# Kernel tuning notes

Hardware: AMD Instinct MI355X
Metric: run time of the kernel (lower is better)

## Reference

```python
import jax, jax.numpy as jnp
import numpy as np

EPS = 1e-5  # torch group_norm default
GROUPS = 32


def _nin(t, W, b):
    # torch Nin: einsum('bchw,co->bowh') transposes spatial dims, then adds bias
    return jnp.einsum('bchw,co->bowh', t, W) + b


def setup_inputs() -> dict:
    key = jax.random.key(0)
    ks = jax.random.split(key, 9)
    B, C, N = 16, 512, 32
    x = jax.random.normal(ks[0], (B, C, N, N), jnp.float32)
    sc = 0.02
    Wq = jax.random.normal(ks[1], (C, C), jnp.float32) * sc
    Wk = jax.random.normal(ks[2], (C, C), jnp.float32) * sc
    Wv = jax.random.normal(ks[3], (C, C), jnp.float32) * sc
    Wn = jax.random.normal(ks[4], (C, C), jnp.float32) * sc
    bq = jnp.zeros((1, C, 1, 1), jnp.float32)
    bk = jnp.zeros((1, C, 1, 1), jnp.float32)
    bv = jnp.zeros((1, C, 1, 1), jnp.float32)
    bn = jnp.zeros((1, C, 1, 1), jnp.float32)
    return {"x": x, "Wq": Wq, "bq": bq, "Wk": Wk, "bk": bk,
            "Wv": Wv, "bv": bv, "Wn": Wn, "bn": bn}


def reference(x, Wq, bq, Wk, bk, Wv, bv, Wn, bn):
    B, C, H, W = x.shape
    # GroupNorm(32) with no affine params
    xg = x.reshape(B, GROUPS, -1)
    mu = xg.mean(-1, keepdims=True)
    var = xg.var(-1, keepdims=True)
    h = ((xg - mu) / jnp.sqrt(var + EPS)).reshape(B, C, H, W)
    # Nin projections -> spatially transposed (B, C, W, H)
    q = _nin(h, Wq, bq)
    k = _nin(h, Wk, bk)
    v = _nin(h, Wv, bv)
    # scores s[b,w1,w2,h1,h2] = sum_c q[b,c,w1,h1] k[b,c,w2,h2] * C^-0.5
    s = jnp.einsum('bcwh,bcWH->bwWhH', q, k) * (C ** -0.5)
    # softmax over flat (h1,h2) blocks exactly as the torch reshape does
    s = jax.nn.softmax(s.reshape(B, H, W, H * W), axis=-1).reshape(B, H, W, H, W)
    # torch.einsum('bHWHW, bcWH -> bcWH', w, v) takes the DIAGONAL over the
    # repeated H and W labels: diag[b,i,j] = s[b,i,j,i,j], then elementwise
    # scales v: out[b,c,w,h] = diag[b,h,w] * v[b,c,w,h]
    i = jnp.arange(H)
    j = jnp.arange(W)
    diag = s[:, i[:, None], j[None, :], i[:, None], j[None, :]]  # (B,H,W)
    h2 = v * jnp.swapaxes(diag, 1, 2)[:, None]  # (B,C,W,H)
    out = _nin(h2, Wn, bn)  # transposes back -> (B,C,H,W)
    return x + out
```

## Files before the change

### kernel.cpp

```cpp
#include <hip/hip_runtime.h>
#include <hip/hip_bf16.h>

typedef __attribute__((ext_vector_type(8))) short short8;
typedef __attribute__((ext_vector_type(4))) float floatx4;

#define MFMA16(a, b, c) __builtin_amdgcn_mfma_f32_16x16x32_bf16((a), (b), (c), 0, 0, 0)
#define WAIT_VM(N) asm volatile("s_waitcnt vmcnt(" #N ")" ::: "memory")
#define BAR() __builtin_amdgcn_s_barrier()

__device__ __forceinline__ short f2bf(float f) {
    union { float f; unsigned u; } x; x.f = f;
    unsigned r = (x.u + 0x7fffu + ((x.u >> 16) & 1u)) >> 16;
    return (short)r;
}
__device__ __forceinline__ float b2f(short s) {
    union { unsigned u; float f; } x; x.u = ((unsigned)(unsigned short)s) << 16; return x.f;
}
__device__ __forceinline__ int swap5(int p) { return ((p & 31) << 5) | (p >> 5); }

__device__ __forceinline__ void gl2lds16(const short* g, short* l) {
    void* gv = const_cast<short*>(g);
    __builtin_amdgcn_global_load_lds((__attribute__((address_space(1))) void*)gv,
                                     (__attribute__((address_space(3))) void*)l,
                                     16, 0, 0);
}

__global__ void prep_w(const float* __restrict__ Wq, const float* __restrict__ Wk,
                       const float* __restrict__ Wv, const float* __restrict__ Wn,
                       short* __restrict__ Wqc, short* __restrict__ Wkc,
                       short* __restrict__ Wvc, short* __restrict__ Wnt) {
    __shared__ float t[32][33];
    int z = blockIdx.z;
    int o0 = blockIdx.x * 32, c0 = blockIdx.y * 32;
    int lx = threadIdx.x, ly = threadIdx.y;
    if (z < 3) {
        const float* src = (z == 0) ? Wq : (z == 1) ? Wk : Wv;
        short* dst = (z == 0) ? Wqc : (z == 1) ? Wkc : Wvc;
        for (int i = ly; i < 32; i += 8) {
            size_t idx = (size_t)(c0 + i) * 512 + o0 + lx;
            dst[idx] = f2bf(src[idx]);
        }
    } else {
        for (int i = ly; i < 32; i += 8) t[i][lx] = Wn[(size_t)(c0 + i) * 512 + o0 + lx];
        __syncthreads();
        for (int i = ly; i < 32; i += 8)
            Wnt[(size_t)(o0 + i) * 512 + c0 + lx] = f2bf(t[lx][i]);
    }
}

__global__ __launch_bounds__(256) void prep_dots(const float* __restrict__ Wq,
                                                 const float* __restrict__ Wk,
                                                 const float* __restrict__ Wn,
                                                 const float* __restrict__ bq,
                                                 const float* __restrict__ bk,
                                                 const float* __restrict__ bv,
                                                 float* __restrict__ UVC) {
    const int bid = blockIdx.x, tid = threadIdx.x;
    if (bid < 128) {
        const int wv = tid >> 6, ln = tid & 63;
        const int t = bid * 4 + wv;
        const float4* wq4 = (const float4*)(Wq + (size_t)t * 512);
        const float4* wk4 = (const float4*)(Wk + (size_t)t * 512);
        const float4* bk4 = (const float4*)bk;
        const float4* bq4 = (const float4*)bq;
        float su = 0.f, sv = 0.f;
#pragma unroll
        for (int j = 0; j < 2; ++j) {
            int i = ln * 2 + j;
            float4 a = wq4[i], b = bk4[i];
            su += a.x * b.x + a.y * b.y + a.z * b.z + a.w * b.w;
            float4 c = wk4[i], d = bq4[i];
            sv += c.x * d.x + c.y * d.y + c.z * d.z + c.w * d.w;
        }
#pragma unroll
        for (int off = 32; off > 0; off >>= 1) {
            su += __shfl_xor(su, off, 64);
            sv += __shfl_xor(sv, off, 64);
        }
        if (ln == 0) { UVC[t] = su; UVC[512 + t] = sv; }
    } else if (bid == 128) {
        if (tid < 64) {
            const float4* a4 = (const float4*)bq;
            const float4* b4 = (const float4*)bk;
            float s = 0.f;
#pragma unroll
            for (int j = 0; j < 2; ++j) {
                int i = tid * 2 + j;
                float4 a = a4[i], b = b4[i];
                s += a.x * b.x + a.y * b.y + a.z * b.z + a.w * b.w;
            }
#pragma unroll
            for (int off = 32; off > 0; off >>= 1) s += __shfl_xor(s, off, 64);
            if (tid == 0) UVC[1024] = s;
        }
    } else {
        const int t = (bid - 129) * 256 + tid;
        float s = 0.f;
        for (int o = 0; o < 512; ++o) s += bv[o] * Wn[(size_t)o * 512 + t];
        UVC[1025 + t] = s;
    }
}

__global__ __launch_bounds__(256) void gemm2(const short* __restrict__ Wkc,
                                             const short* __restrict__ Wqc,
                                             const short* __restrict__ Wnt,
                                             const short* __restrict__ Wvc,
                                             short* __restrict__ Gt,
                                             short* __restrict__ W2t) {
    const int tid = threadIdx.x;
    const int wv = tid >> 6, ln = tid & 63;
    const int z = blockIdx.y;
    const short* A  = (z == 0) ? Wkc : Wnt;
    const short* Wt = (z == 0) ? Wqc : Wvc;
    short* O = (z == 0) ? Gt : W2t;
    const int m0 = (blockIdx.x & 3) * 128, n0 = (blockIdx.x >> 2) * 128;

    __shared__ __attribute__((aligned(16))) short As[3][128 * 32];
    __shared__ __attribute__((aligned(16))) short Bs[3][128 * 32];

    floatx4 acc[4][4] = {};
    const int wm = (wv >> 1) * 64, wn = (wv & 1) * 64;
    const int fr = ln & 15, fq = ln >> 4;

    int sr[2], sq[2];
#pragma unroll
    for (int j = 0; j < 2; ++j) {
        int s = (wv * 2 + j) * 64 + ln;
        sr[j] = s >> 2;
        sq[j] = ((s & 3) ^ ((sr[j] >> 1) & 3)) * 8;
    }
    int aoff[4], boff[4];
#pragma unroll
    for (int t = 0; t < 4; ++t) {
        int ra = wm + t * 16 + fr;
        aoff[t] = ra * 32 + ((fq ^ ((ra >> 1) & 3)) * 8);
        int rb = wn + t * 16 + fr;
        boff[t] = rb * 32 + ((fq ^ ((rb >> 1) & 3)) * 8);
    }

    short* a0 = &As[0][0]; short* a1 = &As[1][0]; short* a2 = &As[2][0];
    short* b0 = &Bs[0][0]; short* b1 = &Bs[1][0]; short* b2 = &Bs[2][0];

#pragma unroll
    for (int j = 0; j < 2; ++j) {
        gl2lds16(A  + (size_t)(m0 + sr[j]) * 512 + sq[j],      a0 + (wv * 2 + j) * 512);
        gl2lds16(Wt + (size_t)(n0 + sr[j]) * 512 + sq[j],      b0 + (wv * 2 + j) * 512);
        gl2lds16(A  + (size_t)(m0 + sr[j]) * 512 + 32 + sq[j], a1 + (wv * 2 + j) * 512);
        gl2lds16(Wt + (size_t)(n0 + sr[j]) * 512 + 32 + sq[j], b1 + (wv * 2 + j) * 512);
    }

    auto compute = [&](const short* Ap, const short* Bp) {
        short8 af[4], bfr[4];
#pragma unroll
        for (int t = 0; t < 4; ++t) {
            af[t]  = *(const short8*)(Ap + aoff[t]);
            bfr[t] = *(const short8*)(Bp + boff[t]);
        }
#pragma unroll
        for (int mt = 0; mt < 4; ++mt)
#pragma unroll
            for (int nt = 0; nt < 4; ++nt)
                acc[mt][nt] = MFMA16(af[mt], bfr[nt], acc[mt][nt]);
    };

    for (int t = 0; t < 14; ++t) {
        int kp = t * 32 + 64;
#pragma unroll
        for (int j = 0; j < 2; ++j) {
            gl2lds16(A  + (size_t)(m0 + sr[j]) * 512 + kp + sq[j], a2 + (wv * 2 + j) * 512);
            gl2lds16(Wt + (size_t)(n0 + sr[j]) * 512 + kp + sq[j], b2 + (wv * 2 + j) * 512);
        }
        WAIT_VM(8);
        BAR();
        compute(a0, b0);
        BAR();
        short* ta = a0; a0 = a1; a1 = a2; a2 = ta;
        short* tb = b0; b0 = b1; b1 = b2; b2 = tb;
    }
    WAIT_VM(4); BAR();
    compute(a0, b0);
    WAIT_VM(0); BAR();
    compute(a1, b1);

#pragma unroll
    for (int mt = 0; mt < 4; ++mt)
#pragma unroll
        for (int nt = 0; nt < 4; ++nt) {
            int n = n0 + wn + nt * 16 + fr;
#pragma unroll
            for (int r = 0; r < 4; ++r) {
                int m = m0 + wm + mt * 16 + fq * 4 + r;
                O[(size_t)m * 512 + n] = f2bf(acc[mt][nt][r]);
            }
        }
}

__global__ __launch_bounds__(256) void groupnorm_k(const float* __restrict__ x,
                                                   short* __restrict__ hnt) {
    int b = blockIdx.x >> 5, g = blockIdx.x & 31;
    const float* xg = x + ((size_t)b * 512 + g * 16) * 1024;
    const float4* xg4 = (const float4*)xg;
    float s = 0.f, ss = 0.f;
    for (int i = threadIdx.x; i < 4096; i += 256) {
        float4 v = xg4[i];
        s  += v.x + v.y + v.z + v.w;
        ss += v.x * v.x + v.y * v.y + v.z * v.z + v.w * v.w;
    }
#pragma unroll
    for (int off = 32; off > 0; off >>= 1) {
        s  += __shfl_down(s,  off, 64);
        ss += __shfl_down(ss, off, 64);
    }
    __shared__ float red[8];
    int w = threadIdx.x >> 6;
    if ((threadIdx.x & 63) == 0) { red[w] = s; red[4 + w] = ss; }
    __syncthreads();
    float S  = red[0] + red[1] + red[2] + red[3];
    float SS = red[4] + red[5] + red[6] + red[7];
    float mean = S * (1.f / 16384.f);
    float var  = SS * (1.f / 16384.f) - mean * mean;
    float rstd = rsqrtf(var + 1e-5f);
    __shared__ __attribute__((aligned(16))) short tile[16 * 1026];
    for (int i = threadIdx.x; i < 4096; i += 256) {
        float4 v = xg4[i];
        int c = i >> 8, p = (i & 255) * 4;
        short* tp = tile + c * 1026 + p;
        tp[0] = f2bf((v.x - mean) * rstd);
        tp[1] = f2bf((v.y - mean) * rstd);
        tp[2] = f2bf((v.z - mean) * rstd);
        tp[3] = f2bf((v.w - mean) * rstd);
    }
    __syncthreads();
    for (int i = threadIdx.x; i < 2048; i += 256) {
        int p = i >> 1, half = i & 1;
        short8 v;
#pragma unroll
        for (int j = 0; j < 8; ++j) v[j] = tile[(half * 8 + j) * 1026 + p];
        *(short8*)(hnt + ((size_t)b * 1024 + p) * 512 + g * 16 + half * 8) = v;
    }
}

__global__ __launch_bounds__(256) void ruv_k(const short* __restrict__ hnt,
                                             const float* __restrict__ UVC,
                                             float* __restrict__ RuP,
                                             float* __restrict__ RvP) {
    const int b = blockIdx.x >> 4, part = blockIdx.x & 15;
    const int wv = threadIdx.x >> 6, ln = threadIdx.x & 63;
    float uc[8], vc[8];
#pragma unroll
    for (int j = 0; j < 8; ++j) { uc[j] = UVC[ln * 8 + j]; vc[j] = UVC[512 + ln * 8 + j]; }
    for (int rr = 0; rr < 16; ++rr) {
        int p = part * 64 + wv * 16 + rr;
        short8 h = *(const short8*)(hnt + ((size_t)b * 1024 + p) * 512 + ln * 8);
        float su = 0.f, sv = 0.f;
#pragma unroll
        for (int j = 0; j < 8; ++j) { float hv = b2f(h[j]); su += hv * uc[j]; sv += hv * vc[j]; }
#pragma unroll
        for (int off = 32; off > 0; off >>= 1) {
            su += __shfl_xor(su, off, 64);
            sv += __shfl_xor(sv, off, 64);
        }
        if (ln == 0) {
            int pp = swap5(p);
            RuP[(size_t)b * 1024 + pp] = su;
            RvP[(size_t)b * 1024 + pp] = sv;
        }
    }
}

__global__ __launch_bounds__(256) void tgemm(const short* __restrict__ A,
                                             const short* __restrict__ Gt,
                                             short* __restrict__ Tp) {
    const int tid = threadIdx.x;
    const int wv = tid >> 6, ln = tid & 63;
    const int fid = blockIdx.x;
    const int xcd = fid & 7, slot = fid >> 3;
    const int bb = (slot >= 32) ? 1 : 0;
    const int w = slot - bb * 32;
    const int batch = xcd * 2 + bb;
    const int m0 = (w & 7) * 128, n0 = (w >> 3) * 128;
    const size_t BS = 1024 * 512;
    const short* Ab = A + (size_t)batch * BS;
    short* Ob = Tp + (size_t)batch * BS;

    __shared__ __attribute__((aligned(16))) short As[3][128 * 32];
    __shared__ __attribute__((aligned(16))) short Bs[3][128 * 32];

    floatx4 acc[4][4] = {};
    const int wm = (wv >> 1) * 64, wn = (wv & 1) * 64;
    const int fr = ln & 15, fq = ln >> 4;

    int sr[2], sq[2];
#pragma unroll
    for (int j = 0; j < 2; ++j) {
        int s = (wv * 2 + j) * 64 + ln;
        sr[j] = s >> 2;
        sq[j] = ((s & 3) ^ ((sr[j] >> 1) & 3)) * 8;
    }
    int aoff[4], boff[4];
#pragma unroll
    for (int t = 0; t < 4; ++t) {
        int ra = wm + t * 16 + fr;
        aoff[t] = ra * 32 + ((fq ^ ((ra >> 1) & 3)) * 8);
        int rb = wn + t * 16 + fr;
        boff[t] = rb * 32 + ((fq ^ ((rb >> 1) & 3)) * 8);
    }

    short* a0 = &As[0][0]; short* a1 = &As[1][0]; short* a2 = &As[2][0];
    short* b0 = &Bs[0][0]; short* b1 = &Bs[1][0]; short* b2 = &Bs[2][0];

#pragma unroll
    for (int j = 0; j < 2; ++j) {
        gl2lds16(Ab + (size_t)(m0 + sr[j]) * 512 + sq[j],      a0 + (wv * 2 + j) * 512);
        gl2lds16(Gt + (size_t)(n0 + sr[j]) * 512 + sq[j],      b0 + (wv * 2 + j) * 512);
        gl2lds16(Ab + (size_t)(m0 + sr[j]) * 512 + 32 + sq[j], a1 + (wv * 2 + j) * 512);
        gl2lds16(Gt + (size_t)(n0 + sr[j]) * 512 + 32 + sq[j], b1 + (wv * 2 + j) * 512);
    }

    auto compute = [&](const short* Ap, const short* Bp) {
        short8 af[4], bfr[4];
#pragma unroll
        for (int t = 0; t < 4; ++t) {
            af[t]  = *(const short8*)(Ap + aoff[t]);
            bfr[t] = *(const short8*)(Bp + boff[t]);
        }
#pragma unroll
        for (int mt = 0; mt < 4; ++mt)
#pragma unroll
            for (int nt = 0; nt < 4; ++nt)
                acc[mt][nt] = MFMA16(af[mt], bfr[nt], acc[mt][nt]);
    };

    for (int t = 0; t < 14; ++t) {
        int kp = t * 32 + 64;
#pragma unroll
        for (int j = 0; j < 2; ++j) {
            gl2lds16(Ab + (size_t)(m0 + sr[j]) * 512 + kp + sq[j], a2 + (wv * 2 + j) * 512);
            gl2lds16(Gt + (size_t)(n0 + sr[j]) * 512 + kp + sq[j], b2 + (wv * 2 + j) * 512);
        }
        WAIT_VM(8);
        BAR();
        compute(a0, b0);
        BAR();
        short* ta = a0; a0 = a1; a1 = a2; a2 = ta;
        short* tb = b0; b0 = b1; b1 = b2; b2 = tb;
    }
    WAIT_VM(4); BAR();
    compute(a0, b0);
    WAIT_VM(0); BAR();
    compute(a1, b1);

#pragma unroll
    for (int mt = 0; mt < 4; ++mt)
#pragma unroll
        for (int nt = 0; nt < 4; ++nt) {
            int n = n0 + wn + nt * 16 + fr;
#pragma unroll
            for (int r = 0; r < 4; ++r) {
                int m = m0 + wm + mt * 16 + fq * 4 + r;
                Ob[(size_t)swap5(m) * 512 + n] = f2bf(acc[mt][nt][r]);
            }
        }
}

__global__ __launch_bounds__(256, 2) void attn_sm(const short* __restrict__ Tp,
                                                  const short* __restrict__ H,
                                                  const float* __restrict__ RuP,
                                                  const float* __restrict__ RvP,
                                                  const float* __restrict__ UVC,
                                                  float* __restrict__ Dm) {
    const int tid = threadIdx.x;
    const int wv = tid >> 6, ln = tid & 63;
    const int fid = blockIdx.x + (blockIdx.y << 3) + blockIdx.z * 32;
    const int xcd = fid & 7, slot = fid >> 3;
    const int bb = (slot >= 32) ? 1 : 0;
    const int w = slot - bb * 32;
    const int b = xcd * 2 + bb;
    const int m0 = (w & 7) * 128, n0 = (w >> 3) * 256;
    const size_t BS = 1024 * 512;
    const short* Tb = Tp + (size_t)b * BS;
    const short* Hb = H + (size_t)b * BS;

    __shared__ __attribute__((aligned(16))) short As[3][128 * 32];
    __shared__ __attribute__((aligned(16))) short Bs[3][256 * 32];

    floatx4 acc[4][8] = {};
    const int wm = (wv >> 1) * 64, wn = (wv & 1) * 128;
    const int fr = ln & 15, fq = ln >> 4;

    const short* pA[2];
    const short* pB[4];
#pragma unroll
    for (int j = 0; j < 2; ++j) {
        int s = (wv * 2 + j) * 64 + ln;
        int r = s >> 2;
        int q = ((s & 3) ^ ((r >> 1) & 3)) * 8;
        pA[j] = Tb + (size_t)(m0 + r) * 512 + q;
    }
#pragma unroll
    for (int j = 0; j < 4; ++j) {
        int s = (wv * 4 + j) * 64 + ln;
        int r = s >> 2;
        int q = ((s & 3) ^ ((r >> 1) & 3)) * 8;
        pB[j] = Hb + (size_t)swap5(n0 + r) * 512 + q;
    }
    int aoff[4], boff[8];
#pragma unroll
    for (int t = 0; t < 4; ++t) {
        int ra = wm + t * 16 + fr;
        aoff[t] = ra * 32 + ((fq ^ ((ra >> 1) & 3)) * 8);
    }
#pragma unroll
    for (int u = 0; u < 8; ++u) {
        int rb = wn + u * 16 + fr;
        boff[u] = rb * 32 + ((fq ^ ((rb >> 1) & 3)) * 8);
    }

    short* a0 = &As[0][0]; short* a1 = &As[1][0]; short* a2 = &As[2][0];
    short* b0 = &Bs[0][0]; short* b1 = &Bs[1][0]; short* b2 = &Bs[2][0];

#pragma unroll
    for (int j = 0; j < 2; ++j) {
        gl2lds16(pA[j],      a0 + (wv * 2 + j) * 512);
        gl2lds16(pA[j] + 32, a1 + (wv * 2 + j) * 512);
    }
#pragma unroll
    for (int j = 0; j < 4; ++j) {
        gl2lds16(pB[j],      b0 + (wv * 4 + j) * 512);
        gl2lds16(pB[j] + 32, b1 + (wv * 4 + j) * 512);
    }

    auto compute = [&](const short* Ap, const short* Bp) {
        short8 af[4], bfr[8];
#pragma unroll
        for (int t = 0; t < 4; ++t) af[t] = *(const short8*)(Ap + aoff[t]);
#pragma unroll
        for (int u = 0; u < 8; ++u) bfr[u] = *(const short8*)(Bp + boff[u]);
#pragma unroll
        for (int mt = 0; mt < 4; ++mt)
#pragma unroll
            for (int nt = 0; nt < 8; ++nt)
                acc[mt][nt] = MFMA16(af[mt], bfr[nt], acc[mt][nt]);
    };

    for (int t = 0; t < 14; ++t) {
        int kp = t * 32 + 64;
#pragma unroll
        for (int j = 0; j < 2; ++j)
            gl2lds16(pA[j] + kp, a2 + (wv * 2 + j) * 512);
#pragma unroll
        for (int j = 0; j < 4; ++j)
            gl2lds16(pB[j] + kp, b2 + (wv * 4 + j) * 512);
        WAIT_VM(12);
        BAR();
        compute(a0, b0);
        BAR();
        short* ta = a0; a0 = a1; a1 = a2; a2 = ta;
        short* tb = b0; b0 = b1; b1 = b2; b2 = tb;
    }
    WAIT_VM(6); BAR();
    compute(a0, b0);
    WAIT_VM(0); BAR();
    compute(a1, b1);

    const float scale = 0.04419417382415922f;
    const float c0v = UVC[1024];
    const int wbase = (m0 + wm) >> 5;
    const int Wbase = (n0 + wn) >> 5;
#pragma unroll
    for (int si = 0; si < 2; ++si) {
#pragma unroll
        for (int sj = 0; sj < 4; ++sj) {
            int wg = wbase + si, Wg = Wbase + sj;
            float tv[16];
            float mx = -3.0e38f;
#pragma unroll
            for (int mi = 0; mi < 2; ++mi) {
                float4 ru4 = *(const float4*)(RuP + (size_t)b * 1024 + m0 + wm + (2 * si + mi) * 16 + fq * 4);
                const float* rup = (const float*)&ru4;
#pragma unroll
                for (int ni = 0; ni < 2; ++ni) {
                    float rvv = RvP[(size_t)b * 1024 + n0 + wn + (2 * sj + ni) * 16 + fr];
#pragma unroll
                    for (int r = 0; r < 4; ++r) {
                        float u = (acc[2 * si + mi][2 * sj + ni][r] + rup[r] + rvv + c0v) * scale;
                        tv[(mi * 2 + ni) * 4 + r] = u;
                        mx = fmaxf(mx, u);
                    }
                }
            }
#pragma unroll
            for (int off = 32; off > 0; off >>= 1) mx = fmaxf(mx, __shfl_xor(mx, off, 64));
            float se = 0.f;
#pragma unroll
            for (int i = 0; i < 16; ++i) se += __expf(tv[i] - mx);
#pragma unroll
            for (int off = 32; off > 0; off >>= 1) se += __shfl_xor(se, off, 64);
            if (fq == ((wg >> 2) & 3) && fr == (Wg & 15)) {
                int mi = wg >> 4, ni = Wg >> 4;
                float numer = tv[(mi * 2 + ni) * 4 + (wg & 3)];
                Dm[((size_t)b * 32 + wg) * 32 + Wg] = __expf(numer - mx) / se;
            }
        }
    }
}

__global__ __launch_bounds__(256) void out_gemm(const short* __restrict__ A,
                                                const short* __restrict__ Wt,
                                                const float* __restrict__ UVC,
                                                const float* __restrict__ Dm,
                                                const float* __restrict__ bnb,
                                                const float* __restrict__ x,
                                                float* __restrict__ out) {
    const int tid = threadIdx.x;
    const int wv = tid >> 6, ln = tid & 63;
    const int fid = blockIdx.x + (blockIdx.y << 3) + blockIdx.z * 32;
    const int xcd = fid & 7, slot = fid >> 3;
    const int bb = (slot >= 32) ? 1 : 0;
    const int w = slot - bb * 32;
    const int b = xcd * 2 + bb;
    const int m0 = (w & 7) * 128, n0 = (w >> 3) * 128;
    const size_t BS = 1024 * 512;
    const short* Ab = A + (size_t)b * BS;

    __shared__ __attribute__((aligned(16))) short As[3][128 * 32];
    __shared__ __attribute__((aligned(16))) short Bs[3][128 * 32];

    floatx4 acc[4][4] = {};
    const int wm = (wv >> 1) * 64, wn = (wv & 1) * 64;
    const int fr = ln & 15, fq = ln >> 4;

    int sr[2], sq[2];
#pragma unroll
    for (int j = 0; j < 2; ++j) {
        int s = (wv * 2 + j) * 64 + ln;
        sr[j] = s >> 2;
        sq[j] = ((s & 3) ^ ((sr[j] >> 1) & 3)) * 8;
    }
    int aoff[4], boff[4];
#pragma unroll
    for (int t = 0; t < 4; ++t) {
        int ra = wm + t * 16 + fr;
        aoff[t] = ra * 32 + ((fq ^ ((ra >> 1) & 3)) * 8);
        int rb = wn + t * 16 + fr;
        boff[t] = rb * 32 + ((fq ^ ((rb >> 1) & 3)) * 8);
    }

    short* a0 = &As[0][0]; short* a1 = &As[1][0]; short* a2 = &As[2][0];
    short* b0 = &Bs[0][0]; short* b1 = &Bs[1][0]; short* b2 = &Bs[2][0];

#pragma unroll
    for (int j = 0; j < 2; ++j) {
        gl2lds16(Ab + (size_t)(m0 + sr[j]) * 512 + sq[j],      a0 + (wv * 2 + j) * 512);
        gl2lds16(Wt + (size_t)(n0 + sr[j]) * 512 + sq[j],      b0 + (wv * 2 + j) * 512);
        gl2lds16(Ab + (size_t)(m0 + sr[j]) * 512 + 32 + sq[j], a1 + (wv * 2 + j) * 512);
        gl2lds16(Wt + (size_t)(n0 + sr[j]) * 512 + 32 + sq[j], b1 + (wv * 2 + j) * 512);
    }

    auto compute = [&](const short* Ap, const short* Bp) {
        short8 af[4], bfr[4];
#pragma unroll
        for (int t = 0; t < 4; ++t) {
            af[t]  = *(const short8*)(Ap + aoff[t]);
            bfr[t] = *(const short8*)(Bp + boff[t]);
        }
#pragma unroll
        for (int mt = 0; mt < 4; ++mt)
#pragma unroll
            for (int nt = 0; nt < 4; ++nt)
                acc[mt][nt] = MFMA16(af[mt], bfr[nt], acc[mt][nt]);
    };

    for (int t = 0; t < 14; ++t) {
        int kp = t * 32 + 64;
#pragma unroll
        for (int j = 0; j < 2; ++j) {
            gl2lds16(Ab + (size_t)(m0 + sr[j]) * 512 + kp + sq[j], a2 + (wv * 2 + j) * 512);
            gl2lds16(Wt + (size_t)(n0 + sr[j]) * 512 + kp + sq[j], b2 + (wv * 2 + j) * 512);
        }
        WAIT_VM(8);
        BAR();
        compute(a0, b0);
        BAR();
        short* ta = a0; a0 = a1; a1 = a2; a2 = ta;
        short* tb = b0; b0 = b1; b1 = b2; b2 = tb;
    }
    WAIT_VM(4); BAR();
    compute(a0, b0);
    WAIT_VM(0); BAR();
    compute(a1, b1);

#pragma unroll
    for (int mt = 0; mt < 4; ++mt) {
        int mbase = m0 + wm + mt * 16 + fq * 4;
        float4 d4 = *(const float4*)(Dm + (size_t)b * 1024 + mbase);
#pragma unroll
        for (int nt = 0; nt < 4; ++nt) {
            int n = n0 + wn + nt * 16 + fr;
            float bvv = bnb[n];
            float w2bn = UVC[1025 + n];
            size_t base = ((size_t)b * 512 + n) * 1024 + mbase;
            float4 x4 = *(const float4*)(x + base);
            float4 o;
            o.x = x4.x + d4.x * (acc[mt][nt][0] + w2bn) + bvv;
            o.y = x4.y + d4.y * (acc[mt][nt][1] + w2bn) + bvv;
            o.z = x4.z + d4.z * (acc[mt][nt][2] + w2bn) + bvv;
            o.w = x4.w + d4.w * (acc[mt][nt][3] + w2bn) + bvv;
            *(float4*)(out + base) = o;
        }
    }
}

extern "C" void kernel_launch(void* const* d_in, const int* in_sizes, int n_in,
                              void* d_out, int out_size, void* d_ws, size_t ws_size,
                              hipStream_t stream) {
    const float* x  = (const float*)d_in[0];
    const float* Wq = (const float*)d_in[1];
    const float* bq = (const float*)d_in[2];
    const float* Wk = (const float*)d_in[3];
    const float* bk = (const float*)d_in[4];
    const float* Wv = (const float*)d_in[5];
    const float* bv = (const float*)d_in[6];
    const float* Wn = (const float*)d_in[7];
    const float* bn = (const float*)d_in[8];
    float* out = (float*)d_out;
    char* ws = (char*)d_ws;

    const size_t WSZ = (size_t)512 * 512 * 2;
    const size_t TSZ = (size_t)16 * 1024 * 512 * 2;
    short* Wqc = (short*)(ws);
    short* Wkc = (short*)(ws + WSZ);
    short* Wvc = (short*)(ws + 2 * WSZ);
    short* Wnt = (short*)(ws + 3 * WSZ);
    short* Gt  = (short*)(ws + 4 * WSZ);
    short* W2t = (short*)(ws + 5 * WSZ);
    float* UVC = (float*)(ws + 6 * WSZ);
    float* RuP = (float*)(ws + 6 * WSZ + 8192);
    float* RvP = (float*)(ws + 6 * WSZ + 8192 + 65536);
    float* Dm  = (float*)(ws + 6 * WSZ + 8192 + 2 * 65536);
    char*  big = ws + 6 * WSZ + 8192 + 3 * 65536;
    short* hnt = (short*)(big);
    short* Tp  = (short*)(big + TSZ);

    prep_w<<<dim3(16, 16, 4), dim3(32, 8), 0, stream>>>(Wq, Wk, Wv, Wn, Wqc, Wkc, Wvc, Wnt);
    prep_dots<<<131, 256, 0, stream>>>(Wq, Wk, Wn, bq, bk, bv, UVC);
    gemm2<<<dim3(16, 2), 256, 0, stream>>>(Wkc, Wqc, Wnt, Wvc, Gt, W2t);
    groupnorm_k<<<512, 256, 0, stream>>>(x, hnt);
    ruv_k<<<256, 256, 0, stream>>>(hnt, UVC, RuP, RvP);
    tgemm<<<512, 256, 0, stream>>>(hnt, Gt, Tp);
    attn_sm<<<dim3(8, 4, 16), 256, 0, stream>>>(Tp, hnt, RuP, RvP, UVC, Dm);
    out_gemm<<<dim3(8, 4, 16), 256, 0, stream>>>(hnt, W2t, UVC, Dm, bn, x, out);
}
```

Before: 216.2 us.

## Split-K the weight-product GEMM and merge weight prep kernels

Merges the weight-cast/transpose kernel and the bias-dot kernel into one launch. It also splits the bias-times-Wn column reduction across four waves with an LDS reduction. The 512x512 weight-product GEMM, which previously ran on only 32 blocks, is split four ways along K into 128 blocks writing fp32 partials, followed by a reduce-and-cast kernel to bf16. This targets low occupancy in the small GEMM and launch overhead, at the cost of extra fp32 partial traffic and an additional launch.

```diff
diff --git a/kernel.cpp b/kernel.cpp
--- a/kernel.cpp
+++ b/kernel.cpp
@@ -25,42 +25,41 @@
                                      16, 0, 0);
 }
 
-__global__ void prep_w(const float* __restrict__ Wq, const float* __restrict__ Wk,
-                       const float* __restrict__ Wv, const float* __restrict__ Wn,
-                       short* __restrict__ Wqc, short* __restrict__ Wkc,
-                       short* __restrict__ Wvc, short* __restrict__ Wnt) {
+__global__ __launch_bounds__(256) void prep_all(const float* __restrict__ Wq,
+                                                const float* __restrict__ Wk,
+                                                const float* __restrict__ Wv,
+                                                const float* __restrict__ Wn,
+                                                const float* __restrict__ bq,
+                                                const float* __restrict__ bk,
+                                                const float* __restrict__ bv,
+                                                short* __restrict__ Wqc, short* __restrict__ Wkc,
+                                                short* __restrict__ Wvc, short* __restrict__ Wnt,
+                                                float* __restrict__ UVC) {
     __shared__ float t[32][33];
-    int z = blockIdx.z;
-    int o0 = blockIdx.x * 32, c0 = blockIdx.y * 32;
-    int lx = threadIdx.x, ly = threadIdx.y;
-    if (z < 3) {
-        const float* src = (z == 0) ? Wq : (z == 1) ? Wk : Wv;
-        short* dst = (z == 0) ? Wqc : (z == 1) ? Wkc : Wvc;
-        for (int i = ly; i < 32; i += 8) {
-            size_t idx = (size_t)(c0 + i) * 512 + o0 + lx;
-            dst[idx] = f2bf(src[idx]);
-        }
-    } else {
-        for (int i = ly; i < 32; i += 8) t[i][lx] = Wn[(size_t)(c0 + i) * 512 + o0 + lx];
-        __syncthreads();
-        for (int i = ly; i < 32; i += 8)
-            Wnt[(size_t)(o0 + i) * 512 + c0 + lx] = f2bf(t[lx][i]);
-    }
-}
-
-__global__ __launch_bounds__(256) void prep_dots(const float* __restrict__ Wq,
-                                                 const float* __restrict__ Wk,
-                                                 const float* __restrict__ Wn,
-                                                 const float* __restrict__ bq,
-                                                 const float* __restrict__ bk,
-                                                 const float* __restrict__ bv,
-                                                 float* __restrict__ UVC) {
+    __shared__ float red2[4][64];
     const int bid = blockIdx.x, tid = threadIdx.x;
-    if (bid < 128) {
+    if (bid < 1024) {
+        int z = bid >> 8, rem = bid & 255;
+        int o0 = (rem & 15) * 32, c0 = (rem >> 4) * 32;
+        int lx = tid & 31, ly = tid >> 5;
+        if (z < 3) {
+            const float* src = (z == 0) ? Wq : (z == 1) ? Wk : Wv;
+            short* dst = (z == 0) ? Wqc : (z == 1) ? Wkc : Wvc;
+            for (int i = ly; i < 32; i += 8) {
+                size_t idx = (size_t)(c0 + i) * 512 + o0 + lx;
+                dst[idx] = f2bf(src[idx]);
+            }
+        } else {
+            for (int i = ly; i < 32; i += 8) t[i][lx] = Wn[(size_t)(c0 + i) * 512 + o0 + lx];
+            __syncthreads();
+            for (int i = ly; i < 32; i += 8)
+                Wnt[(size_t)(o0 + i) * 512 + c0 + lx] = f2bf(t[lx][i]);
+        }
+    } else if (bid < 1152) {
         const int wv = tid >> 6, ln = tid & 63;
-        const int t = bid * 4 + wv;
-        const float4* wq4 = (const float4*)(Wq + (size_t)t * 512);
-        const float4* wk4 = (const float4*)(Wk + (size_t)t * 512);
+        const int r = (bid - 1024) * 4 + wv;
+        const float4* wq4 = (const float4*)(Wq + (size_t)r * 512);
+        const float4* wk4 = (const float4*)(Wk + (size_t)r * 512);
         const float4* bk4 = (const float4*)bk;
         const float4* bq4 = (const float4*)bq;
         float su = 0.f, sv = 0.f;
@@ -77,8 +76,8 @@
             su += __shfl_xor(su, off, 64);
             sv += __shfl_xor(sv, off, 64);
         }
-        if (ln == 0) { UVC[t] = su; UVC[512 + t] = sv; }
-    } else if (bid == 128) {
+        if (ln == 0) { UVC[r] = su; UVC[512 + r] = sv; }
+    } else if (bid == 1152) {
         if (tid < 64) {
             const float4* a4 = (const float4*)bq;
             const float4* b4 = (const float4*)bk;
@@ -94,25 +93,30 @@
             if (tid == 0) UVC[1024] = s;
         }
     } else {
-        const int t = (bid - 129) * 256 + tid;
+        const int j = bid - 1153;
+        const int w = tid >> 6, lt = tid & 63;
+        const int tcol = j * 64 + lt;
         float s = 0.f;
-        for (int o = 0; o < 512; ++o) s += bv[o] * Wn[(size_t)o * 512 + t];
-        UVC[1025 + t] = s;
-    }
-}
-
-__global__ __launch_bounds__(256) void gemm2(const short* __restrict__ Wkc,
-                                             const short* __restrict__ Wqc,
-                                             const short* __restrict__ Wnt,
-                                             const short* __restrict__ Wvc,
-                                             short* __restrict__ Gt,
-                                             short* __restrict__ W2t) {
+        for (int o = w * 128; o < w * 128 + 128; ++o) s += bv[o] * Wn[(size_t)o * 512 + tcol];
+        red2[w][lt] = s;
+        __syncthreads();
+        if (tid < 64)
+            UVC[1025 + j * 64 + tid] = red2[0][tid] + red2[1][tid] + red2[2][tid] + red2[3][tid];
+    }
+}
+
+__global__ __launch_bounds__(256) void gemm2p(const short* __restrict__ Wkc,
+                                              const short* __restrict__ Wqc,
+                                              const short* __restrict__ Wnt,
+                                              const short* __restrict__ Wvc,
+                                              float* __restrict__ Pacc) {
     const int tid = threadIdx.x;
     const int wv = tid >> 6, ln = tid & 63;
-    const int z = blockIdx.y;
+    const int z = blockIdx.z, ksl = blockIdx.y;
+    const int kbase = ksl * 128;
     const short* A  = (z == 0) ? Wkc : Wnt;
     const short* Wt = (z == 0) ? Wqc : Wvc;
-    short* O = (z == 0) ? Gt : W2t;
+    float* P = Pacc + (size_t)(z * 4 + ksl) * 262144;
     const int m0 = (blockIdx.x & 3) * 128, n0 = (blockIdx.x >> 2) * 128;
 
     __shared__ __attribute__((aligned(16))) short As[3][128 * 32];
@@ -143,10 +147,10 @@
 
 #pragma unroll
     for (int j = 0; j < 2; ++j) {
-        gl2lds16(A  + (size_t)(m0 + sr[j]) * 512 + sq[j],      a0 + (wv * 2 + j) * 512);
-        gl2lds16(Wt + (size_t)(n0 + sr[j]) * 512 + sq[j],      b0 + (wv * 2 + j) * 512);
-        gl2lds16(A  + (size_t)(m0 + sr[j]) * 512 + 32 + sq[j], a1 + (wv * 2 + j) * 512);
-        gl2lds16(Wt + (size_t)(n0 + sr[j]) * 512 + 32 + sq[j], b1 + (wv * 2 + j) * 512);
+        gl2lds16(A  + (size_t)(m0 + sr[j]) * 512 + kbase + sq[j],      a0 + (wv * 2 + j) * 512);
+        gl2lds16(Wt + (size_t)(n0 + sr[j]) * 512 + kbase + sq[j],      b0 + (wv * 2 + j) * 512);
+        gl2lds16(A  + (size_t)(m0 + sr[j]) * 512 + kbase + 32 + sq[j], a1 + (wv * 2 + j) * 512);
+        gl2lds16(Wt + (size_t)(n0 + sr[j]) * 512 + kbase + 32 + sq[j], b1 + (wv * 2 + j) * 512);
     }
 
     auto compute = [&](const short* Ap, const short* Bp) {
@@ -163,8 +167,8 @@
                 acc[mt][nt] = MFMA16(af[mt], bfr[nt], acc[mt][nt]);
     };
 
-    for (int t = 0; t < 14; ++t) {
-        int kp = t * 32 + 64;
+    for (int t = 0; t < 2; ++t) {
+        int kp = kbase + t * 32 + 64;
 #pragma unroll
         for (int j = 0; j < 2; ++j) {
             gl2lds16(A  + (size_t)(m0 + sr[j]) * 512 + kp + sq[j], a2 + (wv * 2 + j) * 512);
@@ -190,9 +194,29 @@
 #pragma unroll
             for (int r = 0; r < 4; ++r) {
                 int m = m0 + wm + mt * 16 + fq * 4 + r;
-                O[(size_t)m * 512 + n] = f2bf(acc[mt][nt][r]);
+                P[(size_t)m * 512 + n] = acc[mt][nt][r];
             }
         }
+}
+
+__global__ __launch_bounds__(256) void reduce_cast(const float* __restrict__ Pacc,
+                                                   short* __restrict__ Gt,
+                                                   short* __restrict__ W2t) {
+    const int bid = blockIdx.x, tid = threadIdx.x;
+    const int z = bid >> 8;
+    const int off = (bid & 255) * 1024 + tid * 4;
+    const float* base = Pacc + (size_t)z * 4 * 262144 + off;
+    float4 s0 = *(const float4*)(base);
+    float4 s1 = *(const float4*)(base + 262144);
+    float4 s2 = *(const float4*)(base + 2 * 262144);
+    float4 s3 = *(const float4*)(base + 3 * 262144);
+    short* dst = z ? W2t : Gt;
+    short4 o;
+    o.x = f2bf(s0.x + s1.x + s2.x + s3.x);
+    o.y = f2bf(s0.y + s1.y + s2.y + s3.y);
+    o.z = f2bf(s0.z + s1.z + s2.z + s3.z);
+    o.w = f2bf(s0.w + s1.w + s2.w + s3.w);
+    *(short4*)(dst + off) = o;
 }
 
 __global__ __launch_bounds__(256) void groupnorm_k(const float* __restrict__ x,
@@ -638,13 +662,14 @@
     float* RuP = (float*)(ws + 6 * WSZ + 8192);
     float* RvP = (float*)(ws + 6 * WSZ + 8192 + 65536);
     float* Dm  = (float*)(ws + 6 * WSZ + 8192 + 2 * 65536);
-    char*  big = ws + 6 * WSZ + 8192 + 3 * 65536;
+    float* Pacc = (float*)(ws + 6 * WSZ + 8192 + 3 * 65536);
+    char*  big = ws + 6 * WSZ + 8192 + 3 * 65536 + 8388608;
     short* hnt = (short*)(big);
     short* Tp  = (short*)(big + TSZ);
 
-    prep_w<<<dim3(16, 16, 4), dim3(32, 8), 0, stream>>>(Wq, Wk, Wv, Wn, Wqc, Wkc, Wvc, Wnt);
-    prep_dots<<<131, 256, 0, stream>>>(Wq, Wk, Wn, bq, bk, bv, UVC);
-    gemm2<<<dim3(16, 2), 256, 0, stream>>>(Wkc, Wqc, Wnt, Wvc, Gt, W2t);
+    prep_all<<<1161, 256, 0, stream>>>(Wq, Wk, Wv, Wn, bq, bk, bv, Wqc, Wkc, Wvc, Wnt, UVC);
+    gemm2p<<<dim3(16, 4, 2), 256, 0, stream>>>(Wkc, Wqc, Wnt, Wvc, Pacc);
+    reduce_cast<<<512, 256, 0, stream>>>(Pacc, Gt, W2t);
     groupnorm_k<<<512, 256, 0, stream>>>(x, hnt);
     ruv_k<<<256, 256, 0, stream>>>(hnt, UVC, RuP, RvP);
     tgemm<<<512, 256, 0, stream>>>(hnt, Gt, Tp);
```

Result: faster. 201.7 us (-6.7%).
